# Kernel optimization log

Measured on AMD Instinct MI355X. Metric: run time of the kernel, lower is better.

## Reference

```python
import jax, jax.numpy as jnp
import numpy as np

EMBED = 1024
HEADS = 16


def setup_inputs() -> dict:
    key = jax.random.key(0)
    k1, k2, k3 = jax.random.split(key, 3)
    B, S, D = 2, 2048, EMBED
    x = jax.random.normal(k1, (B, S, D), dtype=jnp.float32)
    # nn.Linear weights: stored as [out, in]; y = x @ W.T
    w_qkv = jax.random.normal(k2, (3 * D, D), dtype=jnp.float32) * (D ** -0.5)
    w_out = jax.random.normal(k3, (D, D), dtype=jnp.float32) * (D ** -0.5)
    return {"x": x, "w_qkv": w_qkv, "w_out": w_out}


def reference(x, w_qkv, w_out):
    B, S, D = x.shape
    H = HEADS
    hd = D // H
    qkv = x @ w_qkv.T                       # [B, S, 3D]
    q, k, v = jnp.split(qkv, 3, axis=-1)
    # 'b l (head k) -> b head l k'
    def heads(t):
        return t.reshape(B, S, H, hd).transpose(0, 2, 1, 3)
    q, k, v = heads(q), heads(k), heads(v)
    scale = hd ** 0.5
    scores = jnp.einsum('bhqd,bhkd->bhqk', q, k) / scale
    probs = jax.nn.softmax(scores, axis=-1)
    out = jnp.einsum('bhqk,bhkd->bhqd', probs, v)  # [B, H, S, hd]
    out = out.transpose(0, 2, 1, 3).reshape(B, S, D)
    return out @ w_out.T
```

## Files before the change

### kernel.cpp

```cpp
#include <hip/hip_runtime.h>

typedef short short8 __attribute__((ext_vector_type(8)));
typedef short short4v __attribute__((ext_vector_type(4)));
typedef float floatx4 __attribute__((ext_vector_type(4)));
typedef unsigned short ushort_t;

#define EMBED 1024
#define HEADS 16
#define HD 64
#define SEQ 2048
#define BATCH 2
#define QSCALE 0.18033688f

__device__ inline ushort_t f2bf(float f) {
    unsigned int u = __float_as_uint(f);
    u += 0x7fff + ((u >> 16) & 1);
    return (ushort_t)(u >> 16);
}

typedef const __attribute__((address_space(1))) unsigned int* gas_t;
typedef __attribute__((address_space(3))) unsigned int* las_t;
__device__ inline void async_copy16(const ushort_t* g, ushort_t* l) {
    __builtin_amdgcn_global_load_lds((gas_t)g, (las_t)l, 16, 0, 0);
}

__global__ void cast3_kernel(const float* __restrict__ a, ushort_t* __restrict__ oa, int na,
                             const float* __restrict__ b, ushort_t* __restrict__ ob, int nb,
                             const float* __restrict__ c, ushort_t* __restrict__ oc, int nc) {
    int idx = (blockIdx.x * blockDim.x + threadIdx.x) * 4;
    const float* in; ushort_t* out;
    if (idx < na)            { in = a;  out = oa; }
    else if (idx < na + nb)  { in = b;  out = ob; idx -= na; }
    else if (idx < na + nb + nc) { in = c; out = oc; idx -= na + nb; }
    else return;
    float4 f = *(const float4*)(in + idx);
    ushort4 o;
    o.x = f2bf(f.x); o.y = f2bf(f.y); o.z = f2bf(f.z); o.w = f2bf(f.w);
    *(ushort4*)(out + idx) = o;
}

#define BM 128
#define BN 128
#define BK 64

template<int MODE>
__launch_bounds__(256, 3)
__global__ void gemm_bt(const ushort_t* __restrict__ A, const ushort_t* __restrict__ B,
                        float* __restrict__ outF,
                        ushort_t* __restrict__ qb, ushort_t* __restrict__ kb,
                        ushort_t* __restrict__ vtb,
                        int M, int N, int K) {
    __shared__ ushort_t As[BM * BK];
    __shared__ ushort_t Bs[BN * BK];
    const int id   = blockIdx.x;
    const int jj   = id >> 3;
    const int bm   = (id & 7) * 4 + (jj & 3);
    const int bn   = jj >> 2;
    const int t    = threadIdx.x;
    const int lane = t & 63;
    const int wave = t >> 6;
    const int wm   = (wave >> 1) * 64;
    const int wn   = (wave & 1) * 64;
    const int m0   = bm * BM;
    const int n0   = bn * BN;
    const int col  = lane & 15;
    const int quad = lane >> 4;

    const int srow = lane >> 3;
    const int sgr  = (lane & 7) ^ (srow & 7);
    const int slot0 = quad ^ (col & 7);

    floatx4 acc[4][4] = {};

    for (int k0 = 0; k0 < K; k0 += BK) {
        for (int half = 0; half < 4; ++half) {
            int row0 = wave * 32 + half * 8;
            int r = row0 + srow;
            async_copy16(A + (size_t)(m0 + r) * K + k0 + sgr * 8, &As[row0 * BK]);
            async_copy16(B + (size_t)(n0 + r) * K + k0 + sgr * 8, &Bs[row0 * BK]);
        }
        __syncthreads();
        short8 a[2][4], b[2][4];
        for (int i = 0; i < 4; ++i) {
            int base = (wm + i * 16 + col) * BK;
            a[0][i] = *(const short8*)(&As[base + slot0 * 8]);
            a[1][i] = *(const short8*)(&As[base + (slot0 ^ 4) * 8]);
        }
        for (int j = 0; j < 4; ++j) {
            int base = (wn + j * 16 + col) * BK;
            b[0][j] = *(const short8*)(&Bs[base + slot0 * 8]);
            b[1][j] = *(const short8*)(&Bs[base + (slot0 ^ 4) * 8]);
        }
        for (int kk = 0; kk < 2; ++kk)
            for (int i = 0; i < 4; ++i)
                for (int j = 0; j < 4; ++j)
                    acc[i][j] = __builtin_amdgcn_mfma_f32_16x16x32_bf16(a[kk][i], b[kk][j], acc[i][j], 0, 0, 0);
        __syncthreads();
    }

    for (int i = 0; i < 4; ++i)
        for (int j = 0; j < 4; ++j) {
            int n = n0 + wn + j * 16 + col;
            int mb = m0 + wm + i * 16 + quad * 4;
            if (MODE == 1) {
                for (int r = 0; r < 4; ++r)
                    outF[(size_t)(mb + r) * N + n] = acc[i][j][r];
            } else {
                int part = n >> 10;
                int within = n & 1023;
                int h = within >> 6, d = within & 63;
                int bb = mb >> 11, s = mb & 2047;
                if (part == 2) {
                    short4v pv;
                    pv.x = (short)f2bf(acc[i][j][0]); pv.y = (short)f2bf(acc[i][j][1]);
                    pv.z = (short)f2bf(acc[i][j][2]); pv.w = (short)f2bf(acc[i][j][3]);
                    *(short4v*)(vtb + (((size_t)bb * HEADS + h) * HD + d) * SEQ + s) = pv;
                } else {
                    ushort_t* dst = (part == 0) ? qb : kb;
                    const float scl = (part == 0) ? QSCALE : 1.0f;
                    for (int r = 0; r < 4; ++r)
                        dst[(((size_t)bb * HEADS + h) * SEQ + s + r) * HD + d] = f2bf(acc[i][j][r] * scl);
                }
            }
        }
}

__launch_bounds__(512, 4)
__global__ void attn_kernel(const ushort_t* __restrict__ qb_, const ushort_t* __restrict__ kb,
                            const ushort_t* __restrict__ vtb, ushort_t* __restrict__ attn) {
    __shared__ __align__(16) ushort_t lds[32768];
    const int id   = blockIdx.x;
    const int jj   = id >> 3;
    const int bh   = (id & 7) * 4 + (jj >> 4);
    const int qblk = jj & 15;
    const int t    = threadIdx.x;
    const int lane = t & 63;
    const int wave = t >> 6;
    const int g    = wave >> 2;
    const int wv   = wave & 3;
    const int col  = lane & 15;
    const int quad = lane >> 4;
    const int q0   = qblk * 128 + wv * 32;
    const int sw   = col & 7;
    const int srow = lane >> 3;
    const int sgr  = lane & 7;

    const ushort_t* Q  = qb_ + (size_t)bh * SEQ * HD;
    const ushort_t* Kp = kb  + (size_t)bh * SEQ * HD;
    const ushort_t* Vt = vtb + (size_t)bh * HD * SEQ;

    ushort_t* Kb0 = &lds[g * 8192];
    ushort_t* Vb0 = &lds[16384 + g * 8192];

    auto stage = [&](int c, int buf) {
        int kt = c << 6;
        #pragma unroll
        for (int inst = 0; inst < 2; ++inst) {
            int row0 = wv * 16 + inst * 8;
            int r = row0 + srow;
            async_copy16(Kp + (size_t)(kt + r) * HD + (sgr ^ (r & 7)) * 8,
                         Kb0 + buf * 4096 + row0 * 64);
            async_copy16(Vt + (size_t)r * SEQ + kt + (sgr ^ (r & 7)) * 8,
                         Vb0 + buf * 4096 + row0 * 64);
        }
    };

    short8 qf[2][2];
    #pragma unroll
    for (int qt = 0; qt < 2; ++qt) {
        qf[qt][0] = *(const short8*)(Q + (size_t)(q0 + qt * 16 + col) * HD + quad * 8);
        qf[qt][1] = *(const short8*)(Q + (size_t)(q0 + qt * 16 + col) * HD + 32 + quad * 8);
    }

    floatx4 acc[2][4] = {};
    float lsum[2] = {0.f, 0.f};

    stage(g, 0);
    __syncthreads();

    for (int i = 0; i < 16; ++i) {
        const int cur = i & 1;
        if (i < 15) stage(2 * (i + 1) + g, cur ^ 1);
        const ushort_t* Kc = Kb0 + cur * 4096;
        const ushort_t* Vc = Vb0 + cur * 4096;

        #pragma unroll
        for (int h = 0; h < 2; ++h) {
            short8 kf[2][2];
            short4v vf[4][2];
            #pragma unroll
            for (int nl = 0; nl < 2; ++nl) {
                int row = (2 * h + nl) * 16 + col;
                kf[nl][0] = *(const short8*)(Kc + row * 64 + ((quad ^ sw) * 8));
                kf[nl][1] = *(const short8*)(Kc + row * 64 + (((4 + quad) ^ sw) * 8));
            }
            #pragma unroll
            for (int dt = 0; dt < 4; ++dt)
                #pragma unroll
                for (int kl = 0; kl < 2; ++kl) {
                    int ks = h * 2 + kl;
                    int row = dt * 16 + col;
                    int slot = (ks * 2 + (quad >> 1)) ^ sw;
                    vf[dt][kl] = *(const short4v*)(Vc + row * 64 + slot * 8 + (quad & 1) * 4);
                }
            #pragma unroll
            for (int qt = 0; qt < 2; ++qt)
                #pragma unroll
                for (int nl = 0; nl < 2; ++nl) {
                    floatx4 z = {};
                    z = __builtin_amdgcn_mfma_f32_16x16x32_bf16(kf[nl][0], qf[qt][0], z, 0, 0, 0);
                    z = __builtin_amdgcn_mfma_f32_16x16x32_bf16(kf[nl][1], qf[qt][1], z, 0, 0, 0);
                    unsigned u0 = __float_as_uint(__builtin_amdgcn_exp2f(z[0]));
                    unsigned u1 = __float_as_uint(__builtin_amdgcn_exp2f(z[1]));
                    unsigned u2 = __float_as_uint(__builtin_amdgcn_exp2f(z[2]));
                    unsigned u3 = __float_as_uint(__builtin_amdgcn_exp2f(z[3]));
                    lsum[qt] += (__uint_as_float(u0 & 0xffff0000u) + __uint_as_float(u1 & 0xffff0000u))
                              + (__uint_as_float(u2 & 0xffff0000u) + __uint_as_float(u3 & 0xffff0000u));
                    uint2 pk;
                    pk.x = __builtin_amdgcn_perm(u1, u0, 0x07060302u);
                    pk.y = __builtin_amdgcn_perm(u3, u2, 0x07060302u);
                    short4v pb = *(short4v*)&pk;
                    #pragma unroll
                    for (int dt = 0; dt < 4; ++dt)
                        acc[qt][dt] = __builtin_amdgcn_mfma_f32_16x16x16bf16_1k(
                            vf[dt][nl], pb, acc[qt][dt], 0, 0, 0);
                }
        }
        __syncthreads();
    }

    float* fs = (float*)lds;
    const int slot = (wave * 64 + lane) * 20;
    floatx4 accK[4];
    float lsK;
    if (g == 0) {
        #pragma unroll
        for (int d = 0; d < 4; ++d) { *(floatx4*)(&fs[slot + d * 4]) = acc[1][d]; accK[d] = acc[0][d]; }
        fs[slot + 16] = lsum[1]; lsK = lsum[0];
    } else {
        #pragma unroll
        for (int d = 0; d < 4; ++d) { *(floatx4*)(&fs[slot + d * 4]) = acc[0][d]; accK[d] = acc[1][d]; }
        fs[slot + 16] = lsum[0]; lsK = lsum[1];
    }
    __syncthreads();
    const int pslot = ((wave ^ 4) * 64 + lane) * 20;
    #pragma unroll
    for (int d = 0; d < 4; ++d)
        accK[d] += *(const floatx4*)(&fs[pslot + d * 4]);
    float s = lsK + fs[pslot + 16];
    s += __shfl_xor(s, 16);
    s += __shfl_xor(s, 32);
    float inv = 1.0f / s;

    int b = bh >> 4, hh = bh & 15;
    int row = q0 + g * 16 + col;
    #pragma unroll
    for (int dt = 0; dt < 4; ++dt) {
        short4v o;
        o.x = (short)f2bf(accK[dt][0] * inv);
        o.y = (short)f2bf(accK[dt][1] * inv);
        o.z = (short)f2bf(accK[dt][2] * inv);
        o.w = (short)f2bf(accK[dt][3] * inv);
        *(short4v*)(attn + ((size_t)b * SEQ + row) * EMBED + hh * HD + dt * 16 + quad * 4) = o;
    }
}

extern "C" void kernel_launch(void* const* d_in, const int* in_sizes, int n_in,
                              void* d_out, int out_size, void* d_ws, size_t ws_size,
                              hipStream_t stream) {
    const float* x     = (const float*)d_in[0];
    const float* w_qkv = (const float*)d_in[1];
    const float* w_out = (const float*)d_in[2];
    float* out = (float*)d_out;

    char* ws = (char*)d_ws;
    size_t off = 0;
    ushort_t* x_bf    = (ushort_t*)(ws + off); off += (size_t)BATCH * SEQ * EMBED * 2;
    ushort_t* wqkv_bf = (ushort_t*)(ws + off); off += (size_t)3 * EMBED * EMBED * 2;
    ushort_t* wout_bf = (ushort_t*)(ws + off); off += (size_t)EMBED * EMBED * 2;
    ushort_t* q_buf   = (ushort_t*)(ws + off); off += (size_t)BATCH * HEADS * SEQ * HD * 2;
    ushort_t* k_buf   = (ushort_t*)(ws + off); off += (size_t)BATCH * HEADS * SEQ * HD * 2;
    ushort_t* vt_buf  = (ushort_t*)(ws + off); off += (size_t)BATCH * HEADS * SEQ * HD * 2;
    ushort_t* attn_bf = (ushort_t*)(ws + off); off += (size_t)BATCH * SEQ * EMBED * 2;

    int n_x = BATCH * SEQ * EMBED, n_wq = 3 * EMBED * EMBED, n_wo = EMBED * EMBED;
    int n_all = n_x + n_wq + n_wo;
    cast3_kernel<<<n_all / 1024, 256, 0, stream>>>(x, x_bf, n_x, w_qkv, wqkv_bf, n_wq,
                                                   w_out, wout_bf, n_wo);

    gemm_bt<0><<<768, 256, 0, stream>>>(
        x_bf, wqkv_bf, nullptr, q_buf, k_buf, vt_buf, BATCH * SEQ, 3 * EMBED, EMBED);

    attn_kernel<<<512, 512, 0, stream>>>(q_buf, k_buf, vt_buf, attn_bf);

    gemm_bt<1><<<256, 256, 0, stream>>>(
        attn_bf, wout_bf, out, nullptr, nullptr, nullptr, BATCH * SEQ, EMBED, EMBED);
}
```

Measured before the change: 181.3 us.

## Compute softmax row sums via MFMA, add setprio, narrow output GEMM tile

The attention kernel now gets the softmax denominator by running an extra MFMA of the probability tile against a ones vector. This replaces the scalar masked adds and the cross-lane shuffles. The MFMA groups are wrapped in s_setprio so matrix work gets issue priority. The output-projection GEMM is templated to a 64-wide N tile and launched with 512 blocks, so the small 256-block launch fills more CUs. The cost is one extra MFMA per P tile, and the B-tile load loop and block indexing are now parameterised.

```diff
diff --git a/kernel.cpp b/kernel.cpp
--- a/kernel.cpp
+++ b/kernel.cpp
@@ -40,10 +40,9 @@
 }
 
 #define BM 128
-#define BN 128
 #define BK 64
 
-template<int MODE>
+template<int MODE, int TBN>
 __launch_bounds__(256, 3)
 __global__ void gemm_bt(const ushort_t* __restrict__ A, const ushort_t* __restrict__ B,
                         float* __restrict__ outF,
@@ -51,7 +50,7 @@
                         ushort_t* __restrict__ vtb,
                         int M, int N, int K) {
     __shared__ ushort_t As[BM * BK];
-    __shared__ ushort_t Bs[BN * BK];
+    __shared__ ushort_t Bs[TBN * BK];
     const int id   = blockIdx.x;
     const int jj   = id >> 3;
     const int bm   = (id & 7) * 4 + (jj & 3);
@@ -60,46 +59,51 @@
     const int lane = t & 63;
     const int wave = t >> 6;
     const int wm   = (wave >> 1) * 64;
-    const int wn   = (wave & 1) * 64;
+    const int wn   = (wave & 1) * (TBN / 2);
     const int m0   = bm * BM;
-    const int n0   = bn * BN;
+    const int n0   = bn * TBN;
     const int col  = lane & 15;
     const int quad = lane >> 4;
+    constexpr int NJ = TBN / 32;
 
     const int srow = lane >> 3;
     const int sgr  = (lane & 7) ^ (srow & 7);
     const int slot0 = quad ^ (col & 7);
 
-    floatx4 acc[4][4] = {};
+    floatx4 acc[4][NJ] = {};
 
     for (int k0 = 0; k0 < K; k0 += BK) {
         for (int half = 0; half < 4; ++half) {
             int row0 = wave * 32 + half * 8;
             int r = row0 + srow;
             async_copy16(A + (size_t)(m0 + r) * K + k0 + sgr * 8, &As[row0 * BK]);
+        }
+        for (int half = 0; half < TBN / 32; ++half) {
+            int row0 = wave * (TBN / 4) + half * 8;
+            int r = row0 + srow;
             async_copy16(B + (size_t)(n0 + r) * K + k0 + sgr * 8, &Bs[row0 * BK]);
         }
         __syncthreads();
-        short8 a[2][4], b[2][4];
+        short8 a[2][4], b[2][NJ];
         for (int i = 0; i < 4; ++i) {
             int base = (wm + i * 16 + col) * BK;
             a[0][i] = *(const short8*)(&As[base + slot0 * 8]);
             a[1][i] = *(const short8*)(&As[base + (slot0 ^ 4) * 8]);
         }
-        for (int j = 0; j < 4; ++j) {
+        for (int j = 0; j < NJ; ++j) {
             int base = (wn + j * 16 + col) * BK;
             b[0][j] = *(const short8*)(&Bs[base + slot0 * 8]);
             b[1][j] = *(const short8*)(&Bs[base + (slot0 ^ 4) * 8]);
         }
         for (int kk = 0; kk < 2; ++kk)
             for (int i = 0; i < 4; ++i)
-                for (int j = 0; j < 4; ++j)
+                for (int j = 0; j < NJ; ++j)
                     acc[i][j] = __builtin_amdgcn_mfma_f32_16x16x32_bf16(a[kk][i], b[kk][j], acc[i][j], 0, 0, 0);
         __syncthreads();
     }
 
     for (int i = 0; i < 4; ++i)
-        for (int j = 0; j < 4; ++j) {
+        for (int j = 0; j < NJ; ++j) {
             int n = n0 + wn + j * 16 + col;
             int mb = m0 + wm + i * 16 + quad * 4;
             if (MODE == 1) {
@@ -172,8 +176,10 @@
         qf[qt][1] = *(const short8*)(Q + (size_t)(q0 + qt * 16 + col) * HD + 32 + quad * 8);
     }
 
+    const short4v onesf = { (short)0x3F80, (short)0x3F80, (short)0x3F80, (short)0x3F80 };
+
     floatx4 acc[2][4] = {};
-    float lsum[2] = {0.f, 0.f};
+    floatx4 accl[2] = {};
 
     stage(g, 0);
     __syncthreads();
@@ -208,26 +214,32 @@
                 #pragma unroll
                 for (int nl = 0; nl < 2; ++nl) {
                     floatx4 z = {};
+                    __builtin_amdgcn_s_setprio(1);
                     z = __builtin_amdgcn_mfma_f32_16x16x32_bf16(kf[nl][0], qf[qt][0], z, 0, 0, 0);
                     z = __builtin_amdgcn_mfma_f32_16x16x32_bf16(kf[nl][1], qf[qt][1], z, 0, 0, 0);
+                    __builtin_amdgcn_s_setprio(0);
                     unsigned u0 = __float_as_uint(__builtin_amdgcn_exp2f(z[0]));
                     unsigned u1 = __float_as_uint(__builtin_amdgcn_exp2f(z[1]));
                     unsigned u2 = __float_as_uint(__builtin_amdgcn_exp2f(z[2]));
                     unsigned u3 = __float_as_uint(__builtin_amdgcn_exp2f(z[3]));
-                    lsum[qt] += (__uint_as_float(u0 & 0xffff0000u) + __uint_as_float(u1 & 0xffff0000u))
-                              + (__uint_as_float(u2 & 0xffff0000u) + __uint_as_float(u3 & 0xffff0000u));
                     uint2 pk;
                     pk.x = __builtin_amdgcn_perm(u1, u0, 0x07060302u);
                     pk.y = __builtin_amdgcn_perm(u3, u2, 0x07060302u);
                     short4v pb = *(short4v*)&pk;
+                    __builtin_amdgcn_s_setprio(1);
+                    accl[qt] = __builtin_amdgcn_mfma_f32_16x16x16bf16_1k(
+                        onesf, pb, accl[qt], 0, 0, 0);
                     #pragma unroll
                     for (int dt = 0; dt < 4; ++dt)
                         acc[qt][dt] = __builtin_amdgcn_mfma_f32_16x16x16bf16_1k(
                             vf[dt][nl], pb, acc[qt][dt], 0, 0, 0);
+                    __builtin_amdgcn_s_setprio(0);
                 }
         }
         __syncthreads();
     }
+
+    float lsum[2] = { accl[0][0], accl[1][0] };
 
     float* fs = (float*)lds;
     const int slot = (wave * 64 + lane) * 20;
@@ -248,8 +260,6 @@
     for (int d = 0; d < 4; ++d)
         accK[d] += *(const floatx4*)(&fs[pslot + d * 4]);
     float s = lsK + fs[pslot + 16];
-    s += __shfl_xor(s, 16);
-    s += __shfl_xor(s, 32);
     float inv = 1.0f / s;
 
     int b = bh >> 4, hh = bh & 15;
@@ -288,11 +298,11 @@
     cast3_kernel<<<n_all / 1024, 256, 0, stream>>>(x, x_bf, n_x, w_qkv, wqkv_bf, n_wq,
                                                    w_out, wout_bf, n_wo);
 
-    gemm_bt<0><<<768, 256, 0, stream>>>(
+    gemm_bt<0, 128><<<768, 256, 0, stream>>>(
         x_bf, wqkv_bf, nullptr, q_buf, k_buf, vt_buf, BATCH * SEQ, 3 * EMBED, EMBED);
 
     attn_kernel<<<512, 512, 0, stream>>>(q_buf, k_buf, vt_buf, attn_bf);
 
-    gemm_bt<1><<<256, 256, 0, stream>>>(
+    gemm_bt<1, 64><<<512, 256, 0, stream>>>(
         attn_bf, wout_bf, out, nullptr, nullptr, nullptr, BATCH * SEQ, EMBED, EMBED);
 }
```

New measurement: 170.7 us. 1.06x faster.
